# Kernel tuning notes

Measured on AMD Instinct MI355X. Metric: run time of the kernel, lower is better.

The kernel has to match this reference:

```python
import jax, jax.numpy as jnp
import numpy as np

N = 4096        # n_nodes
IN = 512        # in_features
HEADS = 8       # n_heads
HID = 64        # n_hidden = out_features // n_heads
SLOPE = 0.2     # leaky relu negative slope


def setup_inputs() -> dict:
    key = jax.random.key(0)
    k1, k2, k3, k4 = jax.random.split(key, 4)
    h = jax.random.normal(k1, (N, IN), dtype=jnp.float32)
    W = jax.random.normal(k2, (IN, HEADS * HID), dtype=jnp.float32) * 0.05
    a = jax.random.normal(k3, (2 * HID,), dtype=jnp.float32) * 0.05
    adj = jax.random.uniform(k4, (N, N)) < 0.01
    adj = adj | jnp.eye(N, dtype=bool)
    return {"h": h, "adj_mat": adj[..., None], "W": W, "a": a}


def reference(h, adj_mat, W, a):
    # g[i, h, f] = per-head projected features
    g = (h @ W).reshape(N, HEADS, HID)
    # attention Linear on concat([g_i, g_j]) splits into two dot products
    a_l, a_r = a[:HID], a[HID:]
    el = jnp.einsum('ihf,f->ih', g, a_l)   # score contribution of target i
    er = jnp.einsum('jhf,f->jh', g, a_r)   # score contribution of source j
    e = el[:, None, :] + er[None, :, :]    # [N, N, HEADS]
    e = jnp.where(e >= 0, e, SLOPE * e)    # LeakyReLU
    e = jnp.where(adj_mat, e, -jnp.inf)    # mask non-edges (adj broadcasts over heads)
    attn = jax.nn.softmax(e, axis=1)       # softmax over source nodes j
    out = jnp.einsum('ijh,jhf->ihf', attn, g)
    return out.reshape(N, HEADS * HID)     # is_concat=True
```

## Files before the change

kernel.cpp:

```cpp
#include <hip/hip_runtime.h>
#include <cstdint>
#include <cstddef>

#define N_NODES 4096
#define IN_DIM  512
#define HEADS   8
#define HID     64
#define OUTF    (HEADS * HID)
#define SLOPE   0.2f
#define MAXD    256
#define MAXD2   128

typedef __bf16 bf16_t;
typedef __attribute__((ext_vector_type(8))) __bf16 bf16x8;
typedef __attribute__((ext_vector_type(4))) float    f32x4;

#define GLD16(gp, lp)                                                                  \
    __builtin_amdgcn_global_load_lds((const __attribute__((address_space(1))) void*)(gp), \
                                     (__attribute__((address_space(3))) void*)(lp), 16, 0, 0)

__device__ __forceinline__ unsigned short to_bf16_u(float x) {
    uint32_t u = __builtin_bit_cast(uint32_t, x);
    u += 0x7fffu + ((u >> 16) & 1u);
    return (unsigned short)(u >> 16);
}
__device__ __forceinline__ float bfbits_to_f(unsigned short b) {
    uint32_t u = ((uint32_t)b) << 16;
    return __builtin_bit_cast(float, u);
}

__global__ __launch_bounds__(256) void prep_conv(const float* __restrict__ h,
                                                 unsigned short* __restrict__ hhi,
                                                 const float* __restrict__ W,
                                                 unsigned short* __restrict__ whiT,
                                                 unsigned short* __restrict__ wloT) {
    const int b = blockIdx.x;
    const int tid = threadIdx.x;
    if (b < 2048) {
        const int t = b * 256 + tid;
        const float4 v = ((const float4*)h)[t];
        ushort4 hi;
        hi.x = to_bf16_u(v.x); hi.y = to_bf16_u(v.y);
        hi.z = to_bf16_u(v.z); hi.w = to_bf16_u(v.w);
        ((ushort4*)hhi)[t] = hi;
    } else {
        const int idx = (b - 2048) * 256 + tid;
        const int c   = idx & 511;
        const int kq  = (idx >> 9) * 4;
        ushort4 hv, lv;
        float w0 = W[(size_t)(kq + 0) * OUTF + c];
        float w1 = W[(size_t)(kq + 1) * OUTF + c];
        float w2 = W[(size_t)(kq + 2) * OUTF + c];
        float w3 = W[(size_t)(kq + 3) * OUTF + c];
        hv.x = to_bf16_u(w0); lv.x = to_bf16_u(w0 - bfbits_to_f(hv.x));
        hv.y = to_bf16_u(w1); lv.y = to_bf16_u(w1 - bfbits_to_f(hv.y));
        hv.z = to_bf16_u(w2); lv.z = to_bf16_u(w2 - bfbits_to_f(hv.z));
        hv.w = to_bf16_u(w3); lv.w = to_bf16_u(w3 - bfbits_to_f(hv.w));
        *(ushort4*)&whiT[(size_t)c * IN_DIM + kq] = hv;
        *(ushort4*)&wloT[(size_t)c * IN_DIM + kq] = lv;
    }
}

__global__ __launch_bounds__(256) void gemm_pack(const bf16_t* __restrict__ Ahi,
                                                 const bf16_t* __restrict__ BhiT,
                                                 const bf16_t* __restrict__ BloT,
                                                 const float* __restrict__ a,
                                                 unsigned short* __restrict__ Gb,
                                                 float* __restrict__ el,
                                                 float* __restrict__ er,
                                                 const int* __restrict__ adj,
                                                 unsigned short* __restrict__ bm16) {
    __shared__ bf16_t As[2][64 * 64];
    __shared__ bf16_t Bh[2][64 * 64];
    __shared__ bf16_t Bl[2][64 * 64];
    __shared__ float  elp[2][64], erp[2][64];

    const int tid = threadIdx.x;

    if (blockIdx.x >= 512) {
        const int t = (blockIdx.x - 512) * 256 + tid;
        const int4* src = (const int4*)adj + (size_t)t * 4;
        const int4 v0 = src[0], v1 = src[1], v2 = src[2], v3 = src[3];
        uint32_t m = 0;
        m |= (v0.x != 0) ? 1u << 0 : 0;  m |= (v0.y != 0) ? 1u << 1 : 0;
        m |= (v0.z != 0) ? 1u << 2 : 0;  m |= (v0.w != 0) ? 1u << 3 : 0;
        m |= (v1.x != 0) ? 1u << 4 : 0;  m |= (v1.y != 0) ? 1u << 5 : 0;
        m |= (v1.z != 0) ? 1u << 6 : 0;  m |= (v1.w != 0) ? 1u << 7 : 0;
        m |= (v2.x != 0) ? 1u << 8 : 0;  m |= (v2.y != 0) ? 1u << 9 : 0;
        m |= (v2.z != 0) ? 1u << 10 : 0; m |= (v2.w != 0) ? 1u << 11 : 0;
        m |= (v3.x != 0) ? 1u << 12 : 0; m |= (v3.y != 0) ? 1u << 13 : 0;
        m |= (v3.z != 0) ? 1u << 14 : 0; m |= (v3.w != 0) ? 1u << 15 : 0;
        bm16[t] = (unsigned short)m;
        return;
    }

    const int wid = tid >> 6;
    const int lane = tid & 63;
    const int head = blockIdx.x & 7;
    const int i0 = (blockIdx.x >> 3) * 64;
    const int j0 = head * 64;
    const int l15 = lane & 15, kq = lane >> 4;

    const int sr0 = wid * 16 + (lane >> 3);
    const int sc  = (lane & 7) ^ (sr0 & 7);
    const size_t aoff = (size_t)(i0 + sr0) * IN_DIM + sc * 8;
    const size_t boff = (size_t)(j0 + sr0) * IN_DIM + sc * 8;
    const int ld0 = wid * 1024 + lane * 8;

    const int wm = wid >> 1, wn = wid & 1;
    int aro[2][2], bro[2][2];
#pragma unroll
    for (int m = 0; m < 2; ++m) {
        const int row = wm * 32 + m * 16 + l15;
#pragma unroll
        for (int ks = 0; ks < 2; ++ks)
            aro[m][ks] = row * 64 + (((ks * 4 + kq) ^ (row & 7)) * 8);
    }
#pragma unroll
    for (int n = 0; n < 2; ++n) {
        const int col = wn * 32 + n * 16 + l15;
#pragma unroll
        for (int ks = 0; ks < 2; ++ks)
            bro[n][ks] = col * 64 + (((ks * 4 + kq) ^ (col & 7)) * 8);
    }

    f32x4 acc[2][2] = {};

    auto stage = [&](int buf, int t) {
        const size_t k0 = (size_t)t * 64;
        GLD16(Ahi  + aoff + k0,                       &As[buf][ld0]);
        GLD16(Ahi  + aoff + (size_t)8 * IN_DIM + k0,  &As[buf][ld0 + 512]);
        GLD16(BhiT + boff + k0,                       &Bh[buf][ld0]);
        GLD16(BhiT + boff + (size_t)8 * IN_DIM + k0,  &Bh[buf][ld0 + 512]);
        GLD16(BloT + boff + k0,                       &Bl[buf][ld0]);
        GLD16(BloT + boff + (size_t)8 * IN_DIM + k0,  &Bl[buf][ld0 + 512]);
    };

    stage(0, 0);
    for (int t = 0; t < 8; ++t) {
        const int cur = t & 1;
        if (t < 7) {
            stage(cur ^ 1, t + 1);
            asm volatile("s_waitcnt vmcnt(6)" ::: "memory");
        } else {
            asm volatile("s_waitcnt vmcnt(0)" ::: "memory");
        }
        __builtin_amdgcn_s_barrier();
        asm volatile("" ::: "memory");

        bf16x8 af[2][2], bh2[2][2], bl2[2][2];
#pragma unroll
        for (int m = 0; m < 2; ++m)
#pragma unroll
            for (int ks = 0; ks < 2; ++ks) af[m][ks] = *(const bf16x8*)&As[cur][aro[m][ks]];
#pragma unroll
        for (int n = 0; n < 2; ++n)
#pragma unroll
            for (int ks = 0; ks < 2; ++ks) {
                bh2[n][ks] = *(const bf16x8*)&Bh[cur][bro[n][ks]];
                bl2[n][ks] = *(const bf16x8*)&Bl[cur][bro[n][ks]];
            }
#pragma unroll
        for (int ks = 0; ks < 2; ++ks)
#pragma unroll
            for (int m = 0; m < 2; ++m)
#pragma unroll
                for (int n = 0; n < 2; ++n) {
                    acc[m][n] = __builtin_amdgcn_mfma_f32_16x16x32_bf16(af[m][ks], bh2[n][ks], acc[m][n], 0, 0, 0);
                    acc[m][n] = __builtin_amdgcn_mfma_f32_16x16x32_bf16(af[m][ks], bl2[n][ks], acc[m][n], 0, 0, 0);
                }

        __builtin_amdgcn_s_barrier();
        asm volatile("" ::: "memory");
    }

#pragma unroll
    for (int m = 0; m < 2; ++m)
#pragma unroll
        for (int n = 0; n < 2; ++n) {
            const int col = j0 + wn * 32 + n * 16 + l15;
#pragma unroll
            for (int q = 0; q < 4; ++q) {
                const int row = i0 + wm * 32 + m * 16 + kq * 4 + q;
                Gb[(size_t)row * OUTF + col] = to_bf16_u(acc[m][n][q]);
            }
        }

    float al[2], arr[2];
#pragma unroll
    for (int n = 0; n < 2; ++n) {
        al[n]  = a[wn * 32 + n * 16 + l15];
        arr[n] = a[64 + wn * 32 + n * 16 + l15];
    }
#pragma unroll
    for (int m = 0; m < 2; ++m)
#pragma unroll
        for (int q = 0; q < 4; ++q) {
            float pe = 0.f, pr = 0.f;
#pragma unroll
            for (int n = 0; n < 2; ++n) {
                const float v = acc[m][n][q];
                pe = fmaf(v, al[n], pe);
                pr = fmaf(v, arr[n], pr);
            }
#pragma unroll
            for (int off = 1; off < 16; off <<= 1) {
                pe += __shfl_xor(pe, off);
                pr += __shfl_xor(pr, off);
            }
            if (l15 == 0) {
                const int lrow = wm * 32 + m * 16 + kq * 4 + q;
                elp[wn][lrow] = pe;
                erp[wn][lrow] = pr;
            }
        }
    __syncthreads();
    if (tid < 64) {
        el[(size_t)(i0 + tid) * HEADS + head] = elp[0][tid] + elp[1][tid];
        er[(size_t)(i0 + tid) * HEADS + head] = erp[0][tid] + erp[1][tid];
    }
}

__global__ __launch_bounds__(512) void gat_attn_wave(const unsigned long long* __restrict__ bm64,
                                                     const unsigned short* __restrict__ Gb,
                                                     const float* __restrict__ el,
                                                     const float* __restrict__ er,
                                                     float* __restrict__ out) {
    __shared__ int   nbr[4][2][MAXD2];
    __shared__ float pw[4][8][MAXD2 + 8];
    __shared__ float red[4][2][OUTF];
    __shared__ float sinv[4][8];
    const int tid = threadIdx.x;
    const int lane = tid & 63;
    const int wid = tid >> 6;
    const int r = wid >> 1, sub = wid & 1;
    const int i = blockIdx.x * 4 + r;

    unsigned long long q = bm64[(size_t)i * 64 + lane];
    const int c = __popcll(q);
    int inc = c;
#pragma unroll
    for (int off = 1; off < 64; off <<= 1) {
        const int t = __shfl_up(inc, off);
        if (lane >= off) inc += t;
    }
    const int deg = min(__shfl(inc, 63), MAXD2);
    int pos = inc - c;
    while (q) {
        const int b = __builtin_ctzll(q);
        q &= q - 1;
        if (pos < MAXD2) nbr[r][sub][pos] = lane * 64 + b;
        ++pos;
    }
    asm volatile("s_waitcnt lgkmcnt(0)" ::: "memory");
    __builtin_amdgcn_wave_barrier();

    const float4 el4 = *(const float4*)(el + (size_t)i * 8 + sub * 4);
    float mx[4] = {-1e30f, -1e30f, -1e30f, -1e30f};
    for (int j = lane; j < deg; j += 64) {
        const int nj = nbr[r][sub][j];
        const float4 er4 = *(const float4*)(er + (size_t)nj * 8 + sub * 4);
        float e[4] = {el4.x + er4.x, el4.y + er4.y, el4.z + er4.z, el4.w + er4.w};
#pragma unroll
        for (int hh = 0; hh < 4; ++hh) {
            e[hh] = (e[hh] >= 0.f) ? e[hh] : SLOPE * e[hh];
            pw[r][sub * 4 + hh][j] = e[hh];
            mx[hh] = fmaxf(mx[hh], e[hh]);
        }
    }
#pragma unroll
    for (int off = 1; off < 64; off <<= 1)
#pragma unroll
        for (int hh = 0; hh < 4; ++hh) mx[hh] = fmaxf(mx[hh], __shfl_xor(mx[hh], off));

    float s4[4] = {};
    for (int j = lane; j < deg; j += 64) {
#pragma unroll
        for (int hh = 0; hh < 4; ++hh) {
            const float pe = __expf(pw[r][sub * 4 + hh][j] - mx[hh]);
            pw[r][sub * 4 + hh][j] = pe;
            s4[hh] += pe;
        }
    }
#pragma unroll
    for (int off = 1; off < 64; off <<= 1)
#pragma unroll
        for (int hh = 0; hh < 4; ++hh) s4[hh] += __shfl_xor(s4[hh], off);
    if (lane == 0) {
#pragma unroll
        for (int hh = 0; hh < 4; ++hh) sinv[r][sub * 4 + hh] = 1.f / s4[hh];
    }
    __syncthreads();

    const int myhead = lane >> 3;
    float a8[8] = {};
    const unsigned short* gl = Gb + lane * 8;
#pragma unroll 4
    for (int j = sub; j < deg; j += 2) {
        const int nj = nbr[r][sub][j];
        const float w = pw[r][myhead][j];
        const uint4 v = *(const uint4*)(gl + (size_t)nj * OUTF);
        a8[0] = fmaf(w, bfbits_to_f((unsigned short)(v.x & 0xffffu)), a8[0]);
        a8[1] = fmaf(w, bfbits_to_f((unsigned short)(v.x >> 16)),     a8[1]);
        a8[2] = fmaf(w, bfbits_to_f((unsigned short)(v.y & 0xffffu)), a8[2]);
        a8[3] = fmaf(w, bfbits_to_f((unsigned short)(v.y >> 16)),     a8[3]);
        a8[4] = fmaf(w, bfbits_to_f((unsigned short)(v.z & 0xffffu)), a8[4]);
        a8[5] = fmaf(w, bfbits_to_f((unsigned short)(v.z >> 16)),     a8[5]);
        a8[6] = fmaf(w, bfbits_to_f((unsigned short)(v.w & 0xffffu)), a8[6]);
        a8[7] = fmaf(w, bfbits_to_f((unsigned short)(v.w >> 16)),     a8[7]);
    }
    float4 lo = {a8[0], a8[1], a8[2], a8[3]};
    float4 hi = {a8[4], a8[5], a8[6], a8[7]};
    *(float4*)&red[r][sub][lane * 8 + 0] = lo;
    *(float4*)&red[r][sub][lane * 8 + 4] = hi;
    __syncthreads();

#pragma unroll
    for (int rr = 0; rr < 4; ++rr) {
        const float v = red[rr][0][tid] + red[rr][1][tid];
        out[(size_t)(blockIdx.x * 4 + rr) * OUTF + tid] = v * sinv[rr][tid >> 6];
    }
}

__global__ __launch_bounds__(256) void gemm_f32(const float* __restrict__ A,
                                                const float* __restrict__ B,
                                                float* __restrict__ C) {
    __shared__ float As[16][68];
    __shared__ float Bs[16][64];
    const int tid = threadIdx.x;
    const int tx = tid & 15, ty = tid >> 4;
    const int i0 = blockIdx.y * 64;
    const int j0 = blockIdx.x * 64;
    const int ar = tid >> 2;
    const int ac = (tid & 3) << 2;
    const int bk = tid >> 4;
    const int bc = (tid & 15) << 2;
    float acc[4][4] = {};
    for (int k0 = 0; k0 < IN_DIM; k0 += 16) {
        const float4 av = *(const float4*)(A + (size_t)(i0 + ar) * IN_DIM + k0 + ac);
        const float4 bv = *(const float4*)(B + (size_t)(k0 + bk) * OUTF + j0 + bc);
        __syncthreads();
        As[ac + 0][ar] = av.x; As[ac + 1][ar] = av.y;
        As[ac + 2][ar] = av.z; As[ac + 3][ar] = av.w;
        *(float4*)&Bs[bk][bc] = bv;
        __syncthreads();
#pragma unroll
        for (int k = 0; k < 16; ++k) {
            const float4 a4 = *(const float4*)&As[k][ty << 2];
            const float4 b4 = *(const float4*)&Bs[k][tx << 2];
            const float am[4] = {a4.x, a4.y, a4.z, a4.w};
            const float bn[4] = {b4.x, b4.y, b4.z, b4.w};
#pragma unroll
            for (int m = 0; m < 4; ++m)
#pragma unroll
                for (int n = 0; n < 4; ++n)
                    acc[m][n] = fmaf(am[m], bn[n], acc[m][n]);
        }
    }
#pragma unroll
    for (int m = 0; m < 4; ++m) {
        float4 v = {acc[m][0], acc[m][1], acc[m][2], acc[m][3]};
        *(float4*)(C + (size_t)(i0 + (ty << 2) + m) * OUTF + j0 + (tx << 2)) = v;
    }
}

__global__ __launch_bounds__(512) void el_er_kernel(const float* __restrict__ g,
                                                    const float* __restrict__ a,
                                                    float* __restrict__ el,
                                                    float* __restrict__ er) {
    const int i = blockIdx.x;
    const int wid = threadIdx.x >> 6;
    const int lane = threadIdx.x & 63;
    const float v = g[(size_t)i * OUTF + wid * HID + lane];
    float pl = v * a[lane];
    float pr = v * a[HID + lane];
#pragma unroll
    for (int off = 1; off < 64; off <<= 1) {
        pl += __shfl_xor(pl, off);
        pr += __shfl_xor(pr, off);
    }
    if (lane == 0) {
        el[(size_t)i * HEADS + wid] = pl;
        er[(size_t)i * HEADS + wid] = pr;
    }
}

__global__ __launch_bounds__(512) void gat_attn_f32(const int* __restrict__ adj,
                                                    const float* __restrict__ g,
                                                    const float* __restrict__ el,
                                                    const float* __restrict__ er,
                                                    float* __restrict__ out) {
    const int i = blockIdx.x;
    const int tid = threadIdx.x;
    const int lane = tid & 63;
    const int wid = tid >> 6;

    __shared__ int   nbr[MAXD];
    __shared__ float p[HEADS][MAXD + 2];
    __shared__ float red[8][256];
    __shared__ float sinv[8];
    __shared__ int   wave_base[8];
    __shared__ int   s_deg;

    const int4* row = (const int4*)(adj + (size_t)i * N_NODES);
    const int4 w0 = row[tid * 2 + 0];
    const int4 w1 = row[tid * 2 + 1];
    uint32_t msk = 0;
    if (w0.x) msk |= 1u;   if (w0.y) msk |= 2u;
    if (w0.z) msk |= 4u;   if (w0.w) msk |= 8u;
    if (w1.x) msk |= 16u;  if (w1.y) msk |= 32u;
    if (w1.z) msk |= 64u;  if (w1.w) msk |= 128u;

    const int c = __popc(msk);
    int inc = c;
#pragma unroll
    for (int off = 1; off < 64; off <<= 1) {
        const int t = __shfl_up(inc, off);
        if (lane >= off) inc += t;
    }
    if (lane == 63) wave_base[wid] = inc;
    __syncthreads();
    if (tid == 0) {
        int run = 0;
#pragma unroll
        for (int w = 0; w < 8; ++w) { const int t = wave_base[w]; wave_base[w] = run; run += t; }
        s_deg = run;
    }
    __syncthreads();
    int pos = wave_base[wid] + inc - c;
#pragma unroll
    for (int b = 0; b < 8; ++b) {
        if (msk & (1u << b)) {
            if (pos < MAXD) nbr[pos] = tid * 8 + b;
            ++pos;
        }
    }
    __syncthreads();
    const int deg = min(s_deg, MAXD);

    const float eli = el[(size_t)i * HEADS + wid];
    float m = -1e30f;
    for (int j = lane; j < deg; j += 64) {
        float e = eli + er[(size_t)nbr[j] * HEADS + wid];
        e = (e >= 0.f) ? e : SLOPE * e;
        p[wid][j] = e;
        m = fmaxf(m, e);
    }
#pragma unroll
    for (int off = 1; off < 64; off <<= 1) m = fmaxf(m, __shfl_xor(m, off));
    float s = 0.f;
    for (int j = lane; j < deg; j += 64) {
        const float pe = __expf(p[wid][j] - m);
        p[wid][j] = pe;
        s += pe;
    }
#pragma unroll
    for (int off = 1; off < 64; off <<= 1) s += __shfl_xor(s, off);
    if (lane == 0) sinv[wid] = 1.f / s;
    __syncthreads();

    const int half = wid >> 2, jslot = wid & 3;
    const int head = half * 4 + (lane >> 4);
    const int f4 = (lane & 15) * 4;
    const float* gbase = g + (size_t)head * HID + f4;
    float4 acc = {0.f, 0.f, 0.f, 0.f};
#pragma unroll 4
    for (int j = jslot; j < deg; j += 4) {
        const int nj = nbr[j];
        const float w = p[head][j];
        const float4 v = *(const float4*)(gbase + (size_t)nj * OUTF);
        acc.x = fmaf(w, v.x, acc.x);
        acc.y = fmaf(w, v.y, acc.y);
        acc.z = fmaf(w, v.z, acc.z);
        acc.w = fmaf(w, v.w, acc.w);
    }
    *(float4*)&red[wid][(lane >> 4) * 64 + f4] = acc;
    __syncthreads();

    const int hf = tid >> 8, loc = tid & 255;
    const float v = red[hf * 4 + 0][loc] + red[hf * 4 + 1][loc] +
                    red[hf * 4 + 2][loc] + red[hf * 4 + 3][loc];
    out[(size_t)i * OUTF + tid] = v * sinv[tid >> 6];
}

extern "C" void kernel_launch(void* const* d_in, const int* in_sizes, int n_in,
                              void* d_out, int out_size, void* d_ws, size_t ws_size,
                              hipStream_t stream) {
    const float* h   = (const float*)d_in[0];
    const int*   adj = (const int*)d_in[1];
    const float* W   = (const float*)d_in[2];
    const float* a   = (const float*)d_in[3];
    float* out = (float*)d_out;
    char* ws = (char*)d_ws;

    const size_t G_OFF   = 0;
    const size_t EL_OFF  = 8388608;
    const size_t ER_OFF  = 8519680;
    const size_t BM_OFF  = 8650752;
    const size_t HHI_OFF = 10747904;
    const size_t WHI_OFF = 14942208;
    const size_t WLO_OFF = 15466496;
    const size_t NEED_FULL = 15990784;

    float* el = (float*)(ws + EL_OFF);
    float* er = (float*)(ws + ER_OFF);

    if (ws_size >= NEED_FULL) {
        unsigned short* gbf  = (unsigned short*)(ws + G_OFF);
        unsigned short* bm   = (unsigned short*)(ws + BM_OFF);
        unsigned short* hhi  = (unsigned short*)(ws + HHI_OFF);
        unsigned short* whiT = (unsigned short*)(ws + WHI_OFF);
        unsigned short* wloT = (unsigned short*)(ws + WLO_OFF);
        prep_conv<<<2304, 256, 0, stream>>>(h, hhi, W, whiT, wloT);
        gemm_pack<<<4608, 256, 0, stream>>>((const bf16_t*)hhi, (const bf16_t*)whiT,
                                            (const bf16_t*)wloT, a, gbf, el, er, adj, bm);
        gat_attn_wave<<<1024, 512, 0, stream>>>((const unsigned long long*)bm, gbf, el, er, out);
    } else {
        float* g = (float*)(ws + G_OFF);
        gemm_f32<<<dim3(8, 64), 256, 0, stream>>>(h, W, g);
        el_er_kernel<<<N_NODES, 512, 0, stream>>>(g, a, el, er);
        gat_attn_f32<<<N_NODES, 512, 0, stream>>>(adj, g, el, er, out);
    }
}
```

Baseline: 43.91 us.

## Load fp32 h directly in GEMM and move adjacency packing into prep kernel

The separate pass that converts h to bf16 is removed. The GEMM now streams fp32 h tiles into LDS with a 16-way swizzle and converts them to bf16 while reading fragments, which saves one global write and read of h. Adjacency bitmask packing moves from the GEMM launch into the prep kernel alongside the W split. As a result the GEMM grid is only the 512 tiles, with head-major block ordering. The trade-offs are doubled LDS and global traffic for the A tile inside the GEMM, extra conversion ALU work, and a larger serial prep kernel that now runs before the GEMM instead of overlapping with it.

```diff
diff --git a/kernel.cpp b/kernel.cpp
--- a/kernel.cpp
+++ b/kernel.cpp
@@ -29,22 +29,29 @@
     return __builtin_bit_cast(float, u);
 }
 
-__global__ __launch_bounds__(256) void prep_conv(const float* __restrict__ h,
-                                                 unsigned short* __restrict__ hhi,
-                                                 const float* __restrict__ W,
-                                                 unsigned short* __restrict__ whiT,
-                                                 unsigned short* __restrict__ wloT) {
+__global__ __launch_bounds__(256) void streampack(const int* __restrict__ adj,
+                                                  unsigned short* __restrict__ bm16,
+                                                  const float* __restrict__ W,
+                                                  unsigned short* __restrict__ whiT,
+                                                  unsigned short* __restrict__ wloT) {
     const int b = blockIdx.x;
     const int tid = threadIdx.x;
-    if (b < 2048) {
+    if (b < 4096) {
         const int t = b * 256 + tid;
-        const float4 v = ((const float4*)h)[t];
-        ushort4 hi;
-        hi.x = to_bf16_u(v.x); hi.y = to_bf16_u(v.y);
-        hi.z = to_bf16_u(v.z); hi.w = to_bf16_u(v.w);
-        ((ushort4*)hhi)[t] = hi;
+        const int4* src = (const int4*)adj + (size_t)t * 4;
+        const int4 v0 = src[0], v1 = src[1], v2 = src[2], v3 = src[3];
+        uint32_t m = 0;
+        m |= (v0.x != 0) ? 1u << 0 : 0;  m |= (v0.y != 0) ? 1u << 1 : 0;
+        m |= (v0.z != 0) ? 1u << 2 : 0;  m |= (v0.w != 0) ? 1u << 3 : 0;
+        m |= (v1.x != 0) ? 1u << 4 : 0;  m |= (v1.y != 0) ? 1u << 5 : 0;
+        m |= (v1.z != 0) ? 1u << 6 : 0;  m |= (v1.w != 0) ? 1u << 7 : 0;
+        m |= (v2.x != 0) ? 1u << 8 : 0;  m |= (v2.y != 0) ? 1u << 9 : 0;
+        m |= (v2.z != 0) ? 1u << 10 : 0; m |= (v2.w != 0) ? 1u << 11 : 0;
+        m |= (v3.x != 0) ? 1u << 12 : 0; m |= (v3.y != 0) ? 1u << 13 : 0;
+        m |= (v3.z != 0) ? 1u << 14 : 0; m |= (v3.w != 0) ? 1u << 15 : 0;
+        bm16[t] = (unsigned short)m;
     } else {
-        const int idx = (b - 2048) * 256 + tid;
+        const int idx = (b - 4096) * 256 + tid;
         const int c   = idx & 511;
         const int kq  = (idx >> 9) * 4;
         ushort4 hv, lv;
@@ -61,60 +68,48 @@
     }
 }
 
-__global__ __launch_bounds__(256) void gemm_pack(const bf16_t* __restrict__ Ahi,
+__global__ __launch_bounds__(256) void gemm_f32A(const float* __restrict__ Hf,
                                                  const bf16_t* __restrict__ BhiT,
                                                  const bf16_t* __restrict__ BloT,
                                                  const float* __restrict__ a,
                                                  unsigned short* __restrict__ Gb,
                                                  float* __restrict__ el,
-                                                 float* __restrict__ er,
-                                                 const int* __restrict__ adj,
-                                                 unsigned short* __restrict__ bm16) {
-    __shared__ bf16_t As[2][64 * 64];
+                                                 float* __restrict__ er) {
+    __shared__ float  As[2][64 * 64];
     __shared__ bf16_t Bh[2][64 * 64];
     __shared__ bf16_t Bl[2][64 * 64];
     __shared__ float  elp[2][64], erp[2][64];
 
     const int tid = threadIdx.x;
-
-    if (blockIdx.x >= 512) {
-        const int t = (blockIdx.x - 512) * 256 + tid;
-        const int4* src = (const int4*)adj + (size_t)t * 4;
-        const int4 v0 = src[0], v1 = src[1], v2 = src[2], v3 = src[3];
-        uint32_t m = 0;
-        m |= (v0.x != 0) ? 1u << 0 : 0;  m |= (v0.y != 0) ? 1u << 1 : 0;
-        m |= (v0.z != 0) ? 1u << 2 : 0;  m |= (v0.w != 0) ? 1u << 3 : 0;
-        m |= (v1.x != 0) ? 1u << 4 : 0;  m |= (v1.y != 0) ? 1u << 5 : 0;
-        m |= (v1.z != 0) ? 1u << 6 : 0;  m |= (v1.w != 0) ? 1u << 7 : 0;
-        m |= (v2.x != 0) ? 1u << 8 : 0;  m |= (v2.y != 0) ? 1u << 9 : 0;
-        m |= (v2.z != 0) ? 1u << 10 : 0; m |= (v2.w != 0) ? 1u << 11 : 0;
-        m |= (v3.x != 0) ? 1u << 12 : 0; m |= (v3.y != 0) ? 1u << 13 : 0;
-        m |= (v3.z != 0) ? 1u << 14 : 0; m |= (v3.w != 0) ? 1u << 15 : 0;
-        bm16[t] = (unsigned short)m;
-        return;
-    }
-
     const int wid = tid >> 6;
     const int lane = tid & 63;
-    const int head = blockIdx.x & 7;
-    const int i0 = (blockIdx.x >> 3) * 64;
+    const int head = blockIdx.x >> 6;
+    const int i0 = (blockIdx.x & 63) * 64;
     const int j0 = head * 64;
     const int l15 = lane & 15, kq = lane >> 4;
 
+    size_t aoff[4];
+#pragma unroll
+    for (int c4 = 0; c4 < 4; ++c4) {
+        const int row = wid * 16 + c4 * 4 + (lane >> 4);
+        const int sc = (lane & 15) ^ (row & 15);
+        aoff[c4] = (size_t)(i0 + row) * IN_DIM + sc * 4;
+    }
     const int sr0 = wid * 16 + (lane >> 3);
-    const int sc  = (lane & 7) ^ (sr0 & 7);
-    const size_t aoff = (size_t)(i0 + sr0) * IN_DIM + sc * 8;
-    const size_t boff = (size_t)(j0 + sr0) * IN_DIM + sc * 8;
-    const int ld0 = wid * 1024 + lane * 8;
+    const int scb = (lane & 7) ^ (sr0 & 7);
+    const size_t boff = (size_t)(j0 + sr0) * IN_DIM + scb * 8;
 
     const int wm = wid >> 1, wn = wid & 1;
-    int aro[2][2], bro[2][2];
+    int aro[2][2][2], bro[2][2];
 #pragma unroll
     for (int m = 0; m < 2; ++m) {
         const int row = wm * 32 + m * 16 + l15;
 #pragma unroll
-        for (int ks = 0; ks < 2; ++ks)
-            aro[m][ks] = row * 64 + (((ks * 4 + kq) ^ (row & 7)) * 8);
+        for (int ks = 0; ks < 2; ++ks) {
+            const int c0 = ks * 8 + kq * 2;
+            aro[m][ks][0] = row * 64 + ((c0 + 0) ^ (row & 15)) * 4;
+            aro[m][ks][1] = row * 64 + ((c0 + 1) ^ (row & 15)) * 4;
+        }
     }
 #pragma unroll
     for (int n = 0; n < 2; ++n) {
@@ -128,12 +123,13 @@
 
     auto stage = [&](int buf, int t) {
         const size_t k0 = (size_t)t * 64;
-        GLD16(Ahi  + aoff + k0,                       &As[buf][ld0]);
-        GLD16(Ahi  + aoff + (size_t)8 * IN_DIM + k0,  &As[buf][ld0 + 512]);
-        GLD16(BhiT + boff + k0,                       &Bh[buf][ld0]);
-        GLD16(BhiT + boff + (size_t)8 * IN_DIM + k0,  &Bh[buf][ld0 + 512]);
-        GLD16(BloT + boff + k0,                       &Bl[buf][ld0]);
-        GLD16(BloT + boff + (size_t)8 * IN_DIM + k0,  &Bl[buf][ld0 + 512]);
+#pragma unroll
+        for (int c4 = 0; c4 < 4; ++c4)
+            GLD16(Hf + aoff[c4] + k0, &As[buf][(wid * 16 + c4 * 4) * 64]);
+        GLD16(BhiT + boff + k0,                      &Bh[buf][(wid * 16) * 64]);
+        GLD16(BhiT + boff + (size_t)8 * IN_DIM + k0, &Bh[buf][(wid * 16 + 8) * 64]);
+        GLD16(BloT + boff + k0,                      &Bl[buf][(wid * 16) * 64]);
+        GLD16(BloT + boff + (size_t)8 * IN_DIM + k0, &Bl[buf][(wid * 16 + 8) * 64]);
     };
 
     stage(0, 0);
@@ -141,18 +137,28 @@
         const int cur = t & 1;
         if (t < 7) {
             stage(cur ^ 1, t + 1);
-            asm volatile("s_waitcnt vmcnt(6)" ::: "memory");
+            asm volatile("s_waitcnt vmcnt(8)" ::: "memory");
         } else {
             asm volatile("s_waitcnt vmcnt(0)" ::: "memory");
         }
         __builtin_amdgcn_s_barrier();
         asm volatile("" ::: "memory");
 
-        bf16x8 af[2][2], bh2[2][2], bl2[2][2];
+        bf16x8 af[2][2];
 #pragma unroll
         for (int m = 0; m < 2; ++m)
 #pragma unroll
-            for (int ks = 0; ks < 2; ++ks) af[m][ks] = *(const bf16x8*)&As[cur][aro[m][ks]];
+            for (int ks = 0; ks < 2; ++ks) {
+                const f32x4 lo4 = *(const f32x4*)&As[cur][aro[m][ks][0]];
+                const f32x4 hi4 = *(const f32x4*)&As[cur][aro[m][ks][1]];
+                bf16x8 v;
+                v[0] = (bf16_t)lo4[0]; v[1] = (bf16_t)lo4[1];
+                v[2] = (bf16_t)lo4[2]; v[3] = (bf16_t)lo4[3];
+                v[4] = (bf16_t)hi4[0]; v[5] = (bf16_t)hi4[1];
+                v[6] = (bf16_t)hi4[2]; v[7] = (bf16_t)hi4[3];
+                af[m][ks] = v;
+            }
+        bf16x8 bh2[2][2], bl2[2][2];
 #pragma unroll
         for (int n = 0; n < 2; ++n)
 #pragma unroll
@@ -493,14 +499,13 @@
     float* out = (float*)d_out;
     char* ws = (char*)d_ws;
 
-    const size_t G_OFF   = 0;
-    const size_t EL_OFF  = 8388608;
-    const size_t ER_OFF  = 8519680;
-    const size_t BM_OFF  = 8650752;
-    const size_t HHI_OFF = 10747904;
-    const size_t WHI_OFF = 14942208;
-    const size_t WLO_OFF = 15466496;
-    const size_t NEED_FULL = 15990784;
+    const size_t G_OFF  = 0;
+    const size_t EL_OFF = 8388608;
+    const size_t ER_OFF = 8519680;
+    const size_t BM_OFF = 8650752;
+    const size_t WHI_OFF = 10747904;
+    const size_t WLO_OFF = 11272192;
+    const size_t NEED_FULL = 11796480;
 
     float* el = (float*)(ws + EL_OFF);
     float* er = (float*)(ws + ER_OFF);
@@ -508,12 +513,11 @@
     if (ws_size >= NEED_FULL) {
         unsigned short* gbf  = (unsigned short*)(ws + G_OFF);
         unsigned short* bm   = (unsigned short*)(ws + BM_OFF);
-        unsigned short* hhi  = (unsigned short*)(ws + HHI_OFF);
         unsigned short* whiT = (unsigned short*)(ws + WHI_OFF);
         unsigned short* wloT = (unsigned short*)(ws + WLO_OFF);
-        prep_conv<<<2304, 256, 0, stream>>>(h, hhi, W, whiT, wloT);
-        gemm_pack<<<4608, 256, 0, stream>>>((const bf16_t*)hhi, (const bf16_t*)whiT,
-                                            (const bf16_t*)wloT, a, gbf, el, er, adj, bm);
+        streampack<<<4352, 256, 0, stream>>>(adj, bm, W, whiT, wloT);
+        gemm_f32A<<<512, 256, 0, stream>>>(h, (const bf16_t*)whiT, (const bf16_t*)wloT,
+                                           a, gbf, el, er);
         gat_attn_wave<<<1024, 512, 0, stream>>>((const unsigned long long*)bm, gbf, el, er, out);
     } else {
         float* g = (float*)(ws + G_OFF);
```

After: 42.90 us. 2.3% less time.
